# Kernel tuning notes

Hardware: AMD Instinct MI355X
Metric: run time of the kernel (lower is better)

The kernel has to match this reference:

```python
import jax, jax.numpy as jnp
import numpy as np

ALPHA = 0.2          # LeakyReLU slope
COUNTER_COEFF = 0.5  # config.counter_coeff
N = 50000
E = 500000
NFEATS = 256
NHIDS = 256
NHEADS = 8
DH = NHIDS // NHEADS


def _gat_multihead(x_src, x_dst, src, dst, W, b, a_s, a_d, a_b, n_dst):
    """Multi-head GAT: gather-linear-leakyrelu edge attention, segment softmax,
    softmax-weighted scatter sum.  W:[H,F,D] b:[H,D] a_s,a_d:[H,D] a_b:[H].
    Returns [n_dst, H*D] (heads concatenated, as torch.cat over heads)."""
    Wh_s = jnp.einsum('nf,hfd->nhd', x_src, W) + b  # [Ns,H,D]
    Wh_d = jnp.einsum('nf,hfd->nhd', x_dst, W) + b  # [Nd,H,D]
    # a([Wh_src;Wh_dst]) decomposes into src and dst halves of the weight
    es = jnp.einsum('nhd,hd->nh', Wh_s, a_s)
    ed = jnp.einsum('nhd,hd->nh', Wh_d, a_d)
    e = jax.nn.leaky_relu(es[src] + ed[dst] + a_b, ALPHA)  # [E,H]
    # per-destination (mailbox) softmax, numerically stable
    emax = jax.ops.segment_max(e, dst, num_segments=n_dst)
    emax = jnp.where(jnp.isfinite(emax), emax, 0.0)
    ex = jnp.exp(e - emax[dst])
    denom = jax.ops.segment_sum(ex, dst, num_segments=n_dst)
    att = ex / denom[dst]                          # every edge's dst has >=1 edge
    msg = att[:, :, None] * Wh_s[src]              # [E,H,D]
    out = jax.ops.segment_sum(msg, dst, num_segments=n_dst)  # [n_dst,H,D]
    return out.reshape(n_dst, -1)


def _gru_cell(x, h, W_ih, W_hh, b_ih, b_hh):
    gi = x @ W_ih.T + b_ih
    gh = h @ W_hh.T + b_hh
    i_r, i_z, i_n = jnp.split(gi, 3, axis=1)
    h_r, h_z, h_n = jnp.split(gh, 3, axis=1)
    r = jax.nn.sigmoid(i_r + h_r)
    z = jax.nn.sigmoid(i_z + h_z)
    n = jnp.tanh(i_n + r * h_n)
    return (1.0 - z) * n + z * h


def setup_inputs() -> dict:
    key = jax.random.key(0)
    ks = jax.random.split(key, 20)
    xavier = lambda k, shape, fin, fout: jax.random.uniform(
        k, shape, jnp.float32, -1.0, 1.0) * (1.414 * np.sqrt(6.0 / (fin + fout)))
    inp = {}
    inp['h'] = jax.random.normal(ks[0], (N, NFEATS), jnp.float32)
    inp['hp_counter'] = jax.random.normal(ks[1], (N, NHIDS), jnp.float32)
    inp['hp_support'] = jax.random.normal(ks[2], (N, NHIDS), jnp.float32)
    inp['hp_dst'] = jax.random.normal(ks[3], (N, NHIDS), jnp.float32)
    # intra-turn GAT weights (per head)
    inp['W_gat'] = xavier(ks[4], (NHEADS, NFEATS, DH), NFEATS, DH)
    inp['b_gat'] = jnp.zeros((NHEADS, DH), jnp.float32)
    inp['as_gat'] = xavier(ks[5], (NHEADS, DH), 2 * DH, 1)
    inp['ad_gat'] = xavier(ks[6], (NHEADS, DH), 2 * DH, 1)
    inp['ab_gat'] = jnp.zeros((NHEADS,), jnp.float32)
    # cross-turn GAT weights (shared for counter & support: same self.xgat)
    inp['W_x'] = xavier(ks[7], (NHEADS, NHIDS, DH), NHIDS, DH)
    inp['b_x'] = jnp.zeros((NHEADS, DH), jnp.float32)
    inp['as_x'] = xavier(ks[8], (NHEADS, DH), 2 * DH, 1)
    inp['ad_x'] = xavier(ks[9], (NHEADS, DH), 2 * DH, 1)
    inp['ab_x'] = jnp.zeros((NHEADS,), jnp.float32)
    # GRUCell(nhids, nhids)
    s = 1.0 / np.sqrt(NHIDS)
    inp['W_ih'] = jax.random.uniform(ks[10], (3 * NHIDS, NHIDS), jnp.float32, -s, s)
    inp['W_hh'] = jax.random.uniform(ks[11], (3 * NHIDS, NHIDS), jnp.float32, -s, s)
    inp['b_ih'] = jax.random.uniform(ks[12], (3 * NHIDS,), jnp.float32, -s, s)
    inp['b_hh'] = jax.random.uniform(ks[13], (3 * NHIDS,), jnp.float32, -s, s)
    # edge lists
    inp['edge_src'] = jax.random.randint(ks[14], (E,), 0, N, jnp.int32)
    inp['edge_dst'] = jax.random.randint(ks[15], (E,), 0, N, jnp.int32)
    inp['edge_c_src'] = jax.random.randint(ks[16], (E,), 0, N, jnp.int32)
    inp['edge_c_dst'] = jax.random.randint(ks[17], (E,), 0, N, jnp.int32)
    inp['edge_s_src'] = jax.random.randint(ks[18], (E,), 0, N, jnp.int32)
    inp['edge_s_dst'] = jax.random.randint(ks[19], (E,), 0, N, jnp.int32)
    return inp


def reference(h, hp_counter, hp_support, hp_dst,
              W_gat, b_gat, as_gat, ad_gat, ab_gat,
              W_x, b_x, as_x, ad_x, ab_x,
              W_ih, W_hh, b_ih, b_hh,
              edge_src, edge_dst, edge_c_src, edge_c_dst,
              edge_s_src, edge_s_dst):
    # x = self.gat(g, t): intra-turn multi-head GAT on raw features h
    x = _gat_multihead(h, h, edge_src, edge_dst,
                       W_gat, b_gat, as_gat, ad_gat, ab_gat, N)
    # h_c = self.xgat(g, t-1, 'counter'): directed GAT, prev-turn -> current
    h_c = _gat_multihead(hp_counter, hp_dst, edge_c_src, edge_c_dst,
                         W_x, b_x, as_x, ad_x, ab_x, N)
    # h_s = self.xgat(g, t-2, 'support') (same weights)
    h_s = _gat_multihead(hp_support, hp_dst, edge_s_src, edge_s_dst,
                         W_x, b_x, as_x, ad_x, ab_x, N)
    hmix = COUNTER_COEFF * h_c + (1.0 - COUNTER_COEFF) * h_s
    hprime = _gru_cell(x, hmix, W_ih, W_hh, b_ih, b_hh)
    return hprime
```

## Files before the change

kernel.cpp:

```cpp
#include <hip/hip_runtime.h>
#include <math.h>

#define ALPHA 0.2f
#define LOG2E 1.44269504088896f

constexpr int FEATS = 256;
constexpr int HEADS = 8;

typedef unsigned short u16;
typedef __attribute__((ext_vector_type(8))) short bf16x8;
typedef __attribute__((ext_vector_type(4))) float f32x4;

__device__ __forceinline__ u16 f2b(float f) {
    unsigned u = __float_as_uint(f);
    u += 0x7FFF + ((u >> 16) & 1);
    return (u16)(u >> 16);
}
__device__ __forceinline__ float b2f(u16 x) {
    return __uint_as_float(((unsigned)x) << 16);
}
__device__ __forceinline__ unsigned pk2(float lo, float hi) {
    return __builtin_amdgcn_perm(__float_as_uint(hi), __float_as_uint(lo), 0x07060302u);
}
__device__ __forceinline__ void gload16(const void* g, void* l) {
    __builtin_amdgcn_global_load_lds(
        (const __attribute__((address_space(1))) unsigned int*)g,
        (__attribute__((address_space(3))) unsigned int*)l, 16, 0, 0);
}
__device__ __forceinline__ float rsum16(float v) {
    v += __shfl_xor(v, 1); v += __shfl_xor(v, 2);
    v += __shfl_xor(v, 4); v += __shfl_xor(v, 8);
    return v;
}

__global__ void prep_count_kernel(
    const float* __restrict__ W_gat, const float* __restrict__ W_x,
    const float* __restrict__ W_ih, const float* __restrict__ W_hh,
    u16* __restrict__ Bgat, u16* __restrict__ Bx,
    u16* __restrict__ Bihr, u16* __restrict__ Bhhr,
    const int* __restrict__ d0, const int* __restrict__ d1,
    const int* __restrict__ d2, int* __restrict__ cnt, int E, int N) {
    int b = blockIdx.x;
    if (b < 2048) {
        int i = b * 256 + threadIdx.x;
        if (i < 131072) {
            int j = i & 65535;
            int n = j >> 8, f = j & 255;
            int h2 = n >> 5, d = n & 31;
            const float* W = (i < 65536) ? W_gat : W_x;
            u16* Bt = (i < 65536) ? Bgat : Bx;
            Bt[j] = f2b(W[(h2 * 256 + f) * 32 + d]);
        } else {
            int x = i - 131072;
            int lin = (x < 196608) ? x : x - 196608;
            int c = lin >> 8, k = lin & 255;
            int q = c / 48, rr = c - q * 48;
            int g = rr >> 4, jl = rr & 15;
            int orig = (g * 256 + q * 16 + jl) * 256 + k;
            if (x < 196608) Bihr[lin] = f2b(W_ih[orig]);
            else            Bhhr[lin] = f2b(W_hh[orig]);
        }
    } else {
        int i = (b - 2048) * 256 + threadIdx.x;
        if (i >= 3 * E) return;
        if (i < E) atomicAdd(&cnt[d0[i]], 1);
        else if (i < 2 * E) atomicAdd(&cnt[N + d1[i - E]], 1);
        else atomicAdd(&cnt[2 * N + d2[i - 2 * E]], 1);
    }
}

__global__ void scan1_kernel(const int* __restrict__ cnt, int* __restrict__ off,
                             int* __restrict__ blksum, int n) {
    __shared__ int tmp[256];
    int t = threadIdx.x;
    int base = blockIdx.x * 1024 + t * 4;
    int v[4];
#pragma unroll
    for (int k = 0; k < 4; ++k) v[k] = (base + k < n) ? cnt[base + k] : 0;
    int s = v[0] + v[1] + v[2] + v[3];
    tmp[t] = s;
    __syncthreads();
    for (int st = 1; st < 256; st <<= 1) {
        int add = (t >= st) ? tmp[t - st] : 0;
        __syncthreads();
        tmp[t] += add;
        __syncthreads();
    }
    int ex = tmp[t] - s;
#pragma unroll
    for (int k = 0; k < 4; ++k) {
        if (base + k < n) off[base + k] = ex;
        ex += v[k];
    }
    if (t == 255) blksum[blockIdx.x] = tmp[255];
}
__global__ void scan2_kernel(int* __restrict__ blksum, int nb) {
    __shared__ int tmp[256];
    int t = threadIdx.x;
    int v = (t < nb) ? blksum[t] : 0;
    tmp[t] = v;
    __syncthreads();
    for (int s = 1; s < 256; s <<= 1) {
        int add = (t >= s) ? tmp[t - s] : 0;
        __syncthreads();
        tmp[t] += add;
        __syncthreads();
    }
    if (t < nb) blksum[t] = tmp[t] - v;
}
__global__ void scan3_kernel(int* __restrict__ off, int* __restrict__ cur,
                             const int* __restrict__ blksum, int n) {
    int i = blockIdx.x * blockDim.x + threadIdx.x;
    if (i < n) {
        int v = off[i] + blksum[i >> 10];
        off[i] = v;
        cur[i] = v;
    }
}

__global__ void fill3_kernel(const int* __restrict__ s0, const int* __restrict__ d0,
                             const int* __restrict__ s1, const int* __restrict__ d1,
                             const int* __restrict__ s2, const int* __restrict__ d2,
                             int* __restrict__ cur, int* __restrict__ srcs, int E, int N) {
    int i = blockIdx.x * blockDim.x + threadIdx.x;
    if (i >= 3 * E) return;
    int s, slot;
    if (i < E) { s = s0[i]; slot = d0[i]; }
    else if (i < 2 * E) { s = s1[i - E]; slot = N + d1[i - E]; }
    else { s = s2[i - 2 * E]; slot = 2 * N + d2[i - 2 * E]; }
    int p = atomicAdd(&cur[slot], 1);
    srcs[p] = s;
}

__global__ __launch_bounds__(512, 4) void proj4_kernel(
    const float* __restrict__ A0, const float* __restrict__ A1,
    const float* __restrict__ A2, const float* __restrict__ A3,
    const u16* __restrict__ Bg, const u16* __restrict__ Bx,
    const float* __restrict__ bg, const float* __restrict__ bx,
    u16* __restrict__ C0, u16* __restrict__ C1,
    u16* __restrict__ C2, u16* __restrict__ C3,
    const float* __restrict__ as_g, const float* __restrict__ ad_g,
    const float* __restrict__ as_x, const float* __restrict__ ad_x,
    float* __restrict__ es1, float* __restrict__ ed1,
    float* __restrict__ esC, float* __restrict__ edD,
    float* __restrict__ esS,
    int M, int NB) {
    __shared__ char As_raw[32768];
    __shared__ char Bs_raw[32768];
    const int tid = threadIdx.x;
    const int lane = tid & 63;
    const int wid = tid >> 6;
    const int wr = wid >> 2, wc = wid & 3;
    const int seg = blockIdx.x / NB;
    const int bm = (blockIdx.x % NB) * 128;
    const int l15 = lane & 15;
    const float* A = (seg == 0) ? A0 : (seg == 1) ? A1 : (seg == 2) ? A2 : A3;
    const u16* B = (seg == 0) ? Bg : Bx;
    const float* bias = (seg == 0) ? bg : bx;
    u16* C = (seg == 0) ? C0 : (seg == 1) ? C1 : (seg == 2) ? C2 : C3;
    const float* asP = (seg == 0) ? as_g : (seg == 2) ? nullptr : as_x;
    const float* adP = (seg == 0) ? ad_g : (seg == 2) ? ad_x : nullptr;
    float* esP = (seg == 0) ? es1 : (seg == 1) ? esC : (seg == 3) ? esS : nullptr;
    float* edP = (seg == 0) ? ed1 : (seg == 2) ? edD : nullptr;

    f32x4 acc[4][4];
#pragma unroll
    for (int m = 0; m < 4; ++m)
#pragma unroll
        for (int n = 0; n < 4; ++n) acc[m][n] = (f32x4)0.f;

    for (int kb = 0; kb < 4; ++kb) {
        const int k0g = kb * 64;
#pragma unroll
        for (int i = 0; i < 4; ++i) {
            int s = i * 512 + tid;
            int row = s >> 4, c16 = s & 15;
            int gr = min(bm + row, M - 1);
            int gcol = k0g + ((c16 ^ (row & 7)) << 2);
            gload16(A + (size_t)gr * 256 + gcol, As_raw + s * 16);
        }
#pragma unroll
        for (int i = 0; i < 4; ++i) {
            int s = i * 512 + tid;
            int row = s >> 3, c16 = s & 7;
            int gcol = k0g + (c16 ^ (row & 7)) * 8;
            gload16(B + (size_t)row * 256 + gcol, Bs_raw + s * 16);
        }
        __syncthreads();
#pragma unroll
        for (int kk = 0; kk < 2; ++kk) {
            const int kc = (kk * 32 + (lane >> 4) * 8) >> 3;
            bf16x8 af[4], bfr[4];
#pragma unroll
            for (int m = 0; m < 4; ++m) {
                int row = wr * 64 + m * 16 + l15;
                int r7 = row & 7;
                int u0 = (2 * kc) ^ r7;
                f32x4 lo = *(const f32x4*)(As_raw + row * 256 + u0 * 16);
                f32x4 hi = *(const f32x4*)(As_raw + row * 256 + (u0 ^ 1) * 16);
                union { unsigned u[4]; bf16x8 v; } cv;
                cv.u[0] = pk2(lo.x, lo.y); cv.u[1] = pk2(lo.z, lo.w);
                cv.u[2] = pk2(hi.x, hi.y); cv.u[3] = pk2(hi.z, hi.w);
                af[m] = cv.v;
            }
#pragma unroll
            for (int n = 0; n < 4; ++n) {
                int row = wc * 64 + n * 16 + l15;
                bfr[n] = *(const bf16x8*)(Bs_raw + row * 128 + ((kc ^ (row & 7)) << 4));
            }
#pragma unroll
            for (int m = 0; m < 4; ++m)
#pragma unroll
                for (int n = 0; n < 4; ++n)
                    acc[m][n] = __builtin_amdgcn_mfma_f32_16x16x32_bf16(
                        af[m], bfr[n], acc[m][n], 0, 0, 0);
        }
        __syncthreads();
    }
    const int hb = wc * 2;
    float cS[4], cD[4];
#pragma unroll
    for (int n = 0; n < 4; ++n) {
        int hn = hb + (n >> 1);
        int ix = (n & 1) * 16 + l15;
        cS[n] = asP ? asP[hn * 32 + ix] : 0.f;
        cD[n] = adP ? adP[hn * 32 + ix] : 0.f;
    }
#pragma unroll
    for (int m = 0; m < 4; ++m) {
#pragma unroll
        for (int j = 0; j < 4; ++j) {
            int gr = bm + wr * 64 + m * 16 + (lane >> 4) * 4 + j;
            float tmp[4];
#pragma unroll
            for (int n = 0; n < 4; ++n)
                tmp[n] = acc[m][n][j] + bias[wc * 64 + n * 16 + l15];
            if (gr < M) {
#pragma unroll
                for (int n = 0; n < 4; ++n)
                    C[(size_t)gr * 256 + wc * 64 + n * 16 + l15] = f2b(tmp[n]);
            }
#pragma unroll
            for (int g = 0; g < 2; ++g) {
                if (esP) {
                    float ps = cS[2 * g] * tmp[2 * g] + cS[2 * g + 1] * tmp[2 * g + 1];
                    ps = rsum16(ps);
                    if (l15 == 0 && gr < M) esP[(size_t)gr * 8 + hb + g] = ps * LOG2E;
                }
                if (edP) {
                    float pd = cD[2 * g] * tmp[2 * g] + cD[2 * g + 1] * tmp[2 * g + 1];
                    pd = rsum16(pd);
                    if (l15 == 0 && gr < M) edP[(size_t)gr * 8 + hb + g] = pd * LOG2E;
                }
            }
        }
    }
}

__device__ __forceinline__ void run_seg(
    const int* __restrict__ srcs, int start, int deg,
    const float* __restrict__ es, const u16* __restrict__ Wh,
    float edv, int o, int hh,
    float& psum, float4& a) {
    psum = 0.f;
    a = make_float4(0.f, 0.f, 0.f, 0.f);
    if (deg <= 0) return;
    int sP = srcs[start];
    int sN = (deg > 1) ? srcs[start + 1] : sP;
    float rawP = es[sP * 8 + hh];
    ushort4 wP = *(const ushort4*)(Wh + (size_t)sP * FEATS + o);
    for (int j = 0; j < deg; ++j) {
        int sNN = (j + 2 < deg) ? srcs[start + j + 2] : sN;
        float rawN = es[sN * 8 + hh];
        ushort4 wN = *(const ushort4*)(Wh + (size_t)sN * FEATS + o);
        float e = rawP + edv;
        e = e > 0.f ? e : ALPHA * e;
        float pe = exp2f(e);
        psum += pe;
        a.x += pe * b2f(wP.x);
        a.y += pe * b2f(wP.y);
        a.z += pe * b2f(wP.z);
        a.w += pe * b2f(wP.w);
        rawP = rawN; wP = wN; sN = sNN;
    }
}

__global__ __launch_bounds__(256) void gather_all_kernel(
    const int* __restrict__ off, const int* __restrict__ cnt,
    const int* __restrict__ srcs,
    const float* __restrict__ es1, const float* __restrict__ ed1,
    const float* __restrict__ esC, const float* __restrict__ edD,
    const float* __restrict__ esS,
    const float* __restrict__ ab_g, const float* __restrict__ ab_x,
    const u16* __restrict__ Wh1, const u16* __restrict__ WhC,
    const u16* __restrict__ WhS3,
    u16* __restrict__ xb, u16* __restrict__ hmixb, int N) {
    int gwid = (blockIdx.x * blockDim.x + threadIdx.x) >> 6;
    if (gwid >= 2 * N) return;
    int lane = threadIdx.x & 63;
    int o = lane * 4, hh = lane >> 3;
    if (gwid < N) {
        int node = gwid;
        float edv = ed1[node * 8 + hh] + ab_g[hh] * LOG2E;
        float psum; float4 a;
        run_seg(srcs, off[node], cnt[node], es1, Wh1, edv, o, hh, psum, a);
        float sc = (cnt[node] > 0) ? (1.0f / psum) : 0.f;
        ushort4 r;
        r.x = f2b(a.x * sc); r.y = f2b(a.y * sc);
        r.z = f2b(a.z * sc); r.w = f2b(a.w * sc);
        *(ushort4*)(xb + (size_t)node * FEATS + o) = r;
    } else {
        int node = gwid - N;
        float edv = edD[node * 8 + hh] + ab_x[hh] * LOG2E;
        int st2 = off[N + node],     dg2 = cnt[N + node];
        int st3 = off[2 * N + node], dg3 = cnt[2 * N + node];
        float ps2, ps3;
        float4 a2, a3;
        if (dg2 > 0 && dg3 > 0) {
            ps2 = 0.f; ps3 = 0.f;
            a2 = make_float4(0.f, 0.f, 0.f, 0.f);
            a3 = make_float4(0.f, 0.f, 0.f, 0.f);
            int sP2 = srcs[st2];
            int sN2 = (dg2 > 1) ? srcs[st2 + 1] : sP2;
            float r2 = esC[sP2 * 8 + hh];
            ushort4 w2 = *(const ushort4*)(WhC + (size_t)sP2 * FEATS + o);
            int sP3 = srcs[st3];
            int sN3 = (dg3 > 1) ? srcs[st3 + 1] : sP3;
            float r3 = esS[sP3 * 8 + hh];
            ushort4 w3 = *(const ushort4*)(WhS3 + (size_t)sP3 * FEATS + o);
            int j2 = 0, j3 = 0;
            const int c = min(dg2, dg3);
            for (int t = 0; t < c; ++t) {
                int sNN2 = (j2 + 2 < dg2) ? srcs[st2 + j2 + 2] : sN2;
                float rn2 = esC[sN2 * 8 + hh];
                ushort4 wn2 = *(const ushort4*)(WhC + (size_t)sN2 * FEATS + o);
                int sNN3 = (j3 + 2 < dg3) ? srcs[st3 + j3 + 2] : sN3;
                float rn3 = esS[sN3 * 8 + hh];
                ushort4 wn3 = *(const ushort4*)(WhS3 + (size_t)sN3 * FEATS + o);
                float e2 = r2 + edv; e2 = e2 > 0.f ? e2 : ALPHA * e2;
                float p2 = exp2f(e2);
                ps2 += p2;
                a2.x += p2 * b2f(w2.x); a2.y += p2 * b2f(w2.y);
                a2.z += p2 * b2f(w2.z); a2.w += p2 * b2f(w2.w);
                float e3 = r3 + edv; e3 = e3 > 0.f ? e3 : ALPHA * e3;
                float p3 = exp2f(e3);
                ps3 += p3;
                a3.x += p3 * b2f(w3.x); a3.y += p3 * b2f(w3.y);
                a3.z += p3 * b2f(w3.z); a3.w += p3 * b2f(w3.w);
                r2 = rn2; w2 = wn2; sN2 = sNN2; ++j2;
                r3 = rn3; w3 = wn3; sN3 = sNN3; ++j3;
            }
            for (; j2 < dg2; ++j2) {
                int sNN2 = (j2 + 2 < dg2) ? srcs[st2 + j2 + 2] : sN2;
                float rn2 = esC[sN2 * 8 + hh];
                ushort4 wn2 = *(const ushort4*)(WhC + (size_t)sN2 * FEATS + o);
                float e2 = r2 + edv; e2 = e2 > 0.f ? e2 : ALPHA * e2;
                float p2 = exp2f(e2);
                ps2 += p2;
                a2.x += p2 * b2f(w2.x); a2.y += p2 * b2f(w2.y);
                a2.z += p2 * b2f(w2.z); a2.w += p2 * b2f(w2.w);
                r2 = rn2; w2 = wn2; sN2 = sNN2;
            }
            for (; j3 < dg3; ++j3) {
                int sNN3 = (j3 + 2 < dg3) ? srcs[st3 + j3 + 2] : sN3;
                float rn3 = esS[sN3 * 8 + hh];
                ushort4 wn3 = *(const ushort4*)(WhS3 + (size_t)sN3 * FEATS + o);
                float e3 = r3 + edv; e3 = e3 > 0.f ? e3 : ALPHA * e3;
                float p3 = exp2f(e3);
                ps3 += p3;
                a3.x += p3 * b2f(w3.x); a3.y += p3 * b2f(w3.y);
                a3.z += p3 * b2f(w3.z); a3.w += p3 * b2f(w3.w);
                r3 = rn3; w3 = wn3; sN3 = sNN3;
            }
        } else {
            run_seg(srcs, st2, dg2, esC, WhC, edv, o, hh, ps2, a2);
            run_seg(srcs, st3, dg3, esS, WhS3, edv, o, hh, ps3, a3);
        }
        float sc2 = (dg2 > 0) ? (0.5f / ps2) : 0.f;
        float sc3 = (dg3 > 0) ? (0.5f / ps3) : 0.f;
        ushort4 r;
        r.x = f2b(a2.x * sc2 + a3.x * sc3);
        r.y = f2b(a2.y * sc2 + a3.y * sc3);
        r.z = f2b(a2.z * sc2 + a3.z * sc3);
        r.w = f2b(a2.w * sc2 + a3.w * sc3);
        *(ushort4*)(hmixb + (size_t)node * FEATS + o) = r;
    }
}

__global__ __launch_bounds__(512, 4) void gru_fused_kernel(
    const u16* __restrict__ xb, const u16* __restrict__ hmixb,
    const u16* __restrict__ Bihr, const u16* __restrict__ Bhhr,
    const float* __restrict__ b_ih, const float* __restrict__ b_hh,
    float* __restrict__ out, int M) {
    __shared__ char As[16384];
    __shared__ char Bs[24576];
    const int tid = threadIdx.x;
    const int lane = tid & 63;
    const int wid = tid >> 6;
    const int wr = wid >> 2, wq = wid & 3;
    const int bt = blockIdx.x;
    const int bm = blockIdx.y * 128;
    const int l15 = lane & 15;

    f32x4 acc[4][3], acc2[4];
#pragma unroll
    for (int m = 0; m < 4; ++m) {
#pragma unroll
        for (int g = 0; g < 3; ++g) acc[m][g] = (f32x4)0.f;
        acc2[m] = (f32x4)0.f;
    }

#pragma unroll
    for (int pass = 0; pass < 2; ++pass) {
        const u16* A = pass ? hmixb : xb;
        const u16* B = pass ? Bhhr : Bihr;
        for (int kb = 0; kb < 4; ++kb) {
            const int k0g = kb * 64;
#pragma unroll
            for (int i = 0; i < 2; ++i) {
                int s = i * 512 + tid;
                int row = s >> 3, c16 = s & 7;
                int gr = min(bm + row, M - 1);
                int gcol = k0g + (c16 ^ (row & 7)) * 8;
                gload16(A + (size_t)gr * 256 + gcol, As + s * 16);
            }
#pragma unroll
            for (int i = 0; i < 3; ++i) {
                int s = i * 512 + tid;
                int row = s >> 3, c16 = s & 7;
                int gcol = k0g + (c16 ^ (row & 7)) * 8;
                gload16(B + (size_t)(bt * 192 + row) * 256 + gcol, Bs + s * 16);
            }
            __syncthreads();
#pragma unroll
            for (int kk = 0; kk < 2; ++kk) {
                const int kc = (kk * 32 + (lane >> 4) * 8) >> 3;
                bf16x8 af[4], bfr[3];
#pragma unroll
                for (int m = 0; m < 4; ++m) {
                    int row = wr * 64 + m * 16 + l15;
                    af[m] = *(const bf16x8*)(As + row * 128 + ((kc ^ (row & 7)) << 4));
                }
#pragma unroll
                for (int g = 0; g < 3; ++g) {
                    int row = wq * 48 + g * 16 + l15;
                    bfr[g] = *(const bf16x8*)(Bs + row * 128 + ((kc ^ (row & 7)) << 4));
                }
#pragma unroll
                for (int m = 0; m < 4; ++m) {
#pragma unroll
                    for (int g = 0; g < 3; ++g) {
                        if (pass == 1 && g == 2)
                            acc2[m] = __builtin_amdgcn_mfma_f32_16x16x32_bf16(
                                af[m], bfr[g], acc2[m], 0, 0, 0);
                        else
                            acc[m][g] = __builtin_amdgcn_mfma_f32_16x16x32_bf16(
                                af[m], bfr[g], acc[m][g], 0, 0, 0);
                    }
                }
            }
            __syncthreads();
        }
    }
    const int j = (bt * 4 + wq) * 16 + l15;
    const float bir = b_ih[j], biz = b_ih[256 + j], bin = b_ih[512 + j];
    const float bhr = b_hh[j], bhz = b_hh[256 + j], bhn = b_hh[512 + j];
#pragma unroll
    for (int m = 0; m < 4; ++m) {
#pragma unroll
        for (int jj = 0; jj < 4; ++jj) {
            int row = bm + wr * 64 + m * 16 + (lane >> 4) * 4 + jj;
            if (row < M) {
                float gr_ = acc[m][0][jj] + bir + bhr;
                float gz_ = acc[m][1][jj] + biz + bhz;
                float rr = 1.f / (1.f + exp2f(-gr_ * LOG2E));
                float zz = 1.f / (1.f + exp2f(-gz_ * LOG2E));
                float nn = tanhf(acc[m][2][jj] + bin + rr * (acc2[m][jj] + bhn));
                float hm = b2f(hmixb[(size_t)row * 256 + j]);
                out[(size_t)row * 256 + j] = (1.f - zz) * nn + zz * hm;
            }
        }
    }
}

extern "C" void kernel_launch(void* const* d_in, const int* in_sizes, int n_in,
                              void* d_out, int out_size, void* d_ws, size_t ws_size,
                              hipStream_t stream) {
    const float* h        = (const float*)d_in[0];
    const float* hp_cnt   = (const float*)d_in[1];
    const float* hp_sup   = (const float*)d_in[2];
    const float* hp_dst   = (const float*)d_in[3];
    const float* W_gat    = (const float*)d_in[4];
    const float* b_gat    = (const float*)d_in[5];
    const float* as_gat   = (const float*)d_in[6];
    const float* ad_gat   = (const float*)d_in[7];
    const float* ab_gat   = (const float*)d_in[8];
    const float* W_x      = (const float*)d_in[9];
    const float* b_x      = (const float*)d_in[10];
    const float* as_x     = (const float*)d_in[11];
    const float* ad_x     = (const float*)d_in[12];
    const float* ab_x     = (const float*)d_in[13];
    const float* W_ih     = (const float*)d_in[14];
    const float* W_hh     = (const float*)d_in[15];
    const float* b_ih     = (const float*)d_in[16];
    const float* b_hh     = (const float*)d_in[17];
    const int* e_src      = (const int*)d_in[18];
    const int* e_dst      = (const int*)d_in[19];
    const int* ec_src     = (const int*)d_in[20];
    const int* ec_dst     = (const int*)d_in[21];
    const int* es_src     = (const int*)d_in[22];
    const int* es_dst     = (const int*)d_in[23];

    const int N = in_sizes[0] / FEATS;
    const int E = in_sizes[18];
    const int N8 = N * HEADS;
    const int N3 = 3 * N;
    const int NBLK3 = (N3 + 1023) / 1024;
    const int NB128 = (N + 127) / 128;

    char* ws = (char*)d_ws;
    size_t p = 0;
    u16* Wh1   = (u16*)(ws + p); p += (size_t)N * FEATS * 2;
    u16* WhC   = (u16*)(ws + p); p += (size_t)N * FEATS * 2;
    u16* WhD   = (u16*)(ws + p); p += (size_t)N * FEATS * 2;
    u16* WhS3  = (u16*)(ws + p); p += (size_t)N * FEATS * 2;
    u16* xb    = (u16*)(ws + p); p += (size_t)N * FEATS * 2;
    u16* hmixb = (u16*)(ws + p); p += (size_t)N * FEATS * 2;
    float* es1 = (float*)(ws + p); p += (size_t)N8 * 4;
    float* ed1 = (float*)(ws + p); p += (size_t)N8 * 4;
    float* esC = (float*)(ws + p); p += (size_t)N8 * 4;
    float* edD = (float*)(ws + p); p += (size_t)N8 * 4;
    float* esS = (float*)(ws + p); p += (size_t)N8 * 4;
    int* cnt3  = (int*)(ws + p); p += (size_t)N3 * 4;
    int* off3  = (int*)(ws + p); p += (size_t)N3 * 4;
    int* cur3  = (int*)(ws + p); p += (size_t)N3 * 4;
    int* blks  = (int*)(ws + p); p += 1024;
    int* srcs3 = (int*)(ws + p); p += (size_t)3 * E * 4;
    u16* Bgat  = (u16*)(ws + p); p += 65536 * 2;
    u16* Bx    = (u16*)(ws + p); p += 65536 * 2;
    u16* Bihr  = (u16*)(ws + p); p += 196608 * 2;
    u16* Bhhr  = (u16*)(ws + p); p += 196608 * 2;

    const dim3 blk(256);
    const dim3 blk512(512);
    const int g3E256 = (3 * E + 255) / 256;

    hipMemsetAsync(cnt3, 0, (size_t)N3 * 4, stream);
    prep_count_kernel<<<2048 + g3E256, blk, 0, stream>>>(
        W_gat, W_x, W_ih, W_hh, Bgat, Bx, Bihr, Bhhr,
        e_dst, ec_dst, es_dst, cnt3, E, N);

    scan1_kernel<<<NBLK3, blk, 0, stream>>>(cnt3, off3, blks, N3);
    scan2_kernel<<<1, blk, 0, stream>>>(blks, NBLK3);
    scan3_kernel<<<(N3 + 255) / 256, blk, 0, stream>>>(off3, cur3, blks, N3);

    fill3_kernel<<<g3E256, blk, 0, stream>>>(e_src, e_dst, ec_src, ec_dst,
                                             es_src, es_dst, cur3, srcs3, E, N);

    proj4_kernel<<<4 * NB128, blk512, 0, stream>>>(
        h, hp_cnt, hp_dst, hp_sup, Bgat, Bx, b_gat, b_x,
        Wh1, WhC, WhD, WhS3,
        as_gat, ad_gat, as_x, ad_x,
        es1, ed1, esC, edD, esS, N, NB128);

    gather_all_kernel<<<(2 * N * 64 + 255) / 256, blk, 0, stream>>>(
        off3, cnt3, srcs3, es1, ed1, esC, edD, esS, ab_gat, ab_x,
        Wh1, WhC, WhS3, xb, hmixb, N);

    gru_fused_kernel<<<dim3(4, NB128), blk512, 0, stream>>>(
        xb, hmixb, Bihr, Bhhr, b_ih, b_hh, (float*)d_out, N);
}
```

Baseline: 484.6 us.

## Double-buffer LDS tiles in projection and GRU GEMMs with K=32 stages

Both GEMM kernels (proj4 and gru_fused) now use two LDS buffers and smaller K-steps of 32. The next tile's global-to-LDS load is issued before computing on the current one, so load latency overlaps with MFMA work and each step needs one barrier instead of two. The swizzle patterns are reworked for the narrower 64/128-byte rows. The trade-off is more loop iterations and barriers with less work per step, plus a changed bank-conflict pattern.

```diff
diff --git a/kernel.cpp b/kernel.cpp
--- a/kernel.cpp
+++ b/kernel.cpp
@@ -145,8 +145,8 @@
     float* __restrict__ esC, float* __restrict__ edD,
     float* __restrict__ esS,
     int M, int NB) {
-    __shared__ char As_raw[32768];
-    __shared__ char Bs_raw[32768];
+    __shared__ char As_raw[2][16384];
+    __shared__ char Bs_raw[2][16384];
     const int tid = threadIdx.x;
     const int lane = tid & 63;
     const int wid = tid >> 6;
@@ -169,52 +169,55 @@
 #pragma unroll
         for (int n = 0; n < 4; ++n) acc[m][n] = (f32x4)0.f;
 
-    for (int kb = 0; kb < 4; ++kb) {
-        const int k0g = kb * 64;
-#pragma unroll
-        for (int i = 0; i < 4; ++i) {
+    auto STAGE = [&](int buf, int kb) {
+        const int k0g = kb * 32;
+#pragma unroll
+        for (int i = 0; i < 2; ++i) {
             int s = i * 512 + tid;
-            int row = s >> 4, c16 = s & 15;
+            int row = s >> 3, c8 = s & 7;
             int gr = min(bm + row, M - 1);
-            int gcol = k0g + ((c16 ^ (row & 7)) << 2);
-            gload16(A + (size_t)gr * 256 + gcol, As_raw + s * 16);
-        }
-#pragma unroll
-        for (int i = 0; i < 4; ++i) {
+            int gcol = k0g + ((c8 ^ (row & 7)) << 2);
+            gload16(A + (size_t)gr * 256 + gcol, As_raw[buf] + s * 16);
+        }
+#pragma unroll
+        for (int i = 0; i < 2; ++i) {
             int s = i * 512 + tid;
-            int row = s >> 3, c16 = s & 7;
-            int gcol = k0g + (c16 ^ (row & 7)) * 8;
-            gload16(B + (size_t)row * 256 + gcol, Bs_raw + s * 16);
-        }
-        __syncthreads();
-#pragma unroll
-        for (int kk = 0; kk < 2; ++kk) {
-            const int kc = (kk * 32 + (lane >> 4) * 8) >> 3;
-            bf16x8 af[4], bfr[4];
-#pragma unroll
-            for (int m = 0; m < 4; ++m) {
-                int row = wr * 64 + m * 16 + l15;
-                int r7 = row & 7;
-                int u0 = (2 * kc) ^ r7;
-                f32x4 lo = *(const f32x4*)(As_raw + row * 256 + u0 * 16);
-                f32x4 hi = *(const f32x4*)(As_raw + row * 256 + (u0 ^ 1) * 16);
-                union { unsigned u[4]; bf16x8 v; } cv;
-                cv.u[0] = pk2(lo.x, lo.y); cv.u[1] = pk2(lo.z, lo.w);
-                cv.u[2] = pk2(hi.x, hi.y); cv.u[3] = pk2(hi.z, hi.w);
-                af[m] = cv.v;
-            }
-#pragma unroll
-            for (int n = 0; n < 4; ++n) {
-                int row = wc * 64 + n * 16 + l15;
-                bfr[n] = *(const bf16x8*)(Bs_raw + row * 128 + ((kc ^ (row & 7)) << 4));
-            }
-#pragma unroll
-            for (int m = 0; m < 4; ++m)
-#pragma unroll
-                for (int n = 0; n < 4; ++n)
-                    acc[m][n] = __builtin_amdgcn_mfma_f32_16x16x32_bf16(
-                        af[m], bfr[n], acc[m][n], 0, 0, 0);
-        }
+            int row = s >> 2, c4 = s & 3;
+            int gcol = k0g + (c4 ^ ((row >> 1) & 3)) * 8;
+            gload16(B + (size_t)row * 256 + gcol, Bs_raw[buf] + s * 16);
+        }
+    };
+
+    STAGE(0, 0);
+    __syncthreads();
+    for (int kb = 0; kb < 8; ++kb) {
+        const int cur = kb & 1;
+        if (kb < 7) STAGE(cur ^ 1, kb + 1);
+        const int kc = lane >> 4;
+        bf16x8 af[4], bfr[4];
+#pragma unroll
+        for (int m = 0; m < 4; ++m) {
+            int row = wr * 64 + m * 16 + l15;
+            int u0 = (2 * kc) ^ (row & 7);
+            f32x4 lo = *(const f32x4*)(As_raw[cur] + row * 128 + u0 * 16);
+            f32x4 hi = *(const f32x4*)(As_raw[cur] + row * 128 + (u0 ^ 1) * 16);
+            union { unsigned u[4]; bf16x8 v; } cv;
+            cv.u[0] = pk2(lo.x, lo.y); cv.u[1] = pk2(lo.z, lo.w);
+            cv.u[2] = pk2(hi.x, hi.y); cv.u[3] = pk2(hi.z, hi.w);
+            af[m] = cv.v;
+        }
+#pragma unroll
+        for (int n = 0; n < 4; ++n) {
+            int row = wc * 64 + n * 16 + l15;
+            bfr[n] = *(const bf16x8*)(Bs_raw[cur] + row * 64 +
+                                      ((kc ^ ((row >> 1) & 3)) << 4));
+        }
+#pragma unroll
+        for (int m = 0; m < 4; ++m)
+#pragma unroll
+            for (int n = 0; n < 4; ++n)
+                acc[m][n] = __builtin_amdgcn_mfma_f32_16x16x32_bf16(
+                    af[m], bfr[n], acc[m][n], 0, 0, 0);
         __syncthreads();
     }
     const int hb = wc * 2;
@@ -392,8 +395,8 @@
     const u16* __restrict__ Bihr, const u16* __restrict__ Bhhr,
     const float* __restrict__ b_ih, const float* __restrict__ b_hh,
     float* __restrict__ out, int M) {
-    __shared__ char As[16384];
-    __shared__ char Bs[24576];
+    __shared__ char As[2][8192];
+    __shared__ char Bs[2][12288];
     const int tid = threadIdx.x;
     const int lane = tid & 63;
     const int wid = tid >> 6;
@@ -410,57 +413,62 @@
         acc2[m] = (f32x4)0.f;
     }
 
-#pragma unroll
-    for (int pass = 0; pass < 2; ++pass) {
+    auto STAGE = [&](int buf, int t) {
+        const int pass = t >> 3, kb = t & 7;
         const u16* A = pass ? hmixb : xb;
         const u16* B = pass ? Bhhr : Bihr;
-        for (int kb = 0; kb < 4; ++kb) {
-            const int k0g = kb * 64;
-#pragma unroll
-            for (int i = 0; i < 2; ++i) {
-                int s = i * 512 + tid;
-                int row = s >> 3, c16 = s & 7;
-                int gr = min(bm + row, M - 1);
-                int gcol = k0g + (c16 ^ (row & 7)) * 8;
-                gload16(A + (size_t)gr * 256 + gcol, As + s * 16);
-            }
-#pragma unroll
-            for (int i = 0; i < 3; ++i) {
-                int s = i * 512 + tid;
-                int row = s >> 3, c16 = s & 7;
-                int gcol = k0g + (c16 ^ (row & 7)) * 8;
-                gload16(B + (size_t)(bt * 192 + row) * 256 + gcol, Bs + s * 16);
-            }
-            __syncthreads();
-#pragma unroll
-            for (int kk = 0; kk < 2; ++kk) {
-                const int kc = (kk * 32 + (lane >> 4) * 8) >> 3;
-                bf16x8 af[4], bfr[3];
-#pragma unroll
-                for (int m = 0; m < 4; ++m) {
-                    int row = wr * 64 + m * 16 + l15;
-                    af[m] = *(const bf16x8*)(As + row * 128 + ((kc ^ (row & 7)) << 4));
-                }
-#pragma unroll
-                for (int g = 0; g < 3; ++g) {
-                    int row = wq * 48 + g * 16 + l15;
-                    bfr[g] = *(const bf16x8*)(Bs + row * 128 + ((kc ^ (row & 7)) << 4));
-                }
-#pragma unroll
-                for (int m = 0; m < 4; ++m) {
-#pragma unroll
-                    for (int g = 0; g < 3; ++g) {
-                        if (pass == 1 && g == 2)
-                            acc2[m] = __builtin_amdgcn_mfma_f32_16x16x32_bf16(
-                                af[m], bfr[g], acc2[m], 0, 0, 0);
-                        else
-                            acc[m][g] = __builtin_amdgcn_mfma_f32_16x16x32_bf16(
-                                af[m], bfr[g], acc[m][g], 0, 0, 0);
-                    }
-                }
-            }
-            __syncthreads();
-        }
+        const int k0g = kb * 32;
+        {
+            int s = tid;
+            int row = s >> 2, c4 = s & 3;
+            int gr = min(bm + row, M - 1);
+            int gcol = k0g + (c4 ^ ((row >> 1) & 3)) * 8;
+            gload16(A + (size_t)gr * 256 + gcol, As[buf] + s * 16);
+        }
+#pragma unroll
+        for (int i = 0; i < 2; ++i) {
+            int s = i * 512 + tid;
+            if (s < 768) {
+                int row = s >> 2, c4 = s & 3;
+                int gcol = k0g + (c4 ^ ((row >> 1) & 3)) * 8;
+                gload16(B + (size_t)(bt * 192 + row) * 256 + gcol, Bs[buf] + s * 16);
+            }
+        }
+    };
+
+    STAGE(0, 0);
+    __syncthreads();
+    for (int t = 0; t < 16; ++t) {
+        const int cur = t & 1;
+        if (t < 15) STAGE(cur ^ 1, t + 1);
+        const int pass = t >> 3;
+        const int kc = lane >> 4;
+        bf16x8 af[4], bfr[3];
+#pragma unroll
+        for (int m = 0; m < 4; ++m) {
+            int row = wr * 64 + m * 16 + l15;
+            af[m] = *(const bf16x8*)(As[cur] + row * 64 +
+                                     ((kc ^ ((row >> 1) & 3)) << 4));
+        }
+#pragma unroll
+        for (int g = 0; g < 3; ++g) {
+            int row = wq * 48 + g * 16 + l15;
+            bfr[g] = *(const bf16x8*)(Bs[cur] + row * 64 +
+                                      ((kc ^ ((row >> 1) & 3)) << 4));
+        }
+#pragma unroll
+        for (int m = 0; m < 4; ++m) {
+#pragma unroll
+            for (int g = 0; g < 3; ++g) {
+                if (pass == 1 && g == 2)
+                    acc2[m] = __builtin_amdgcn_mfma_f32_16x16x32_bf16(
+                        af[m], bfr[g], acc2[m], 0, 0, 0);
+                else
+                    acc[m][g] = __builtin_amdgcn_mfma_f32_16x16x32_bf16(
+                        af[m], bfr[g], acc[m][g], 0, 0, 0);
+            }
+        }
+        __syncthreads();
     }
     const int j = (bt * 4 + wq) * 16 + l15;
     const float bir = b_ih[j], biz = b_ih[256 + j], bin = b_ih[512 + j];
```

Measured after the change: 486.7 us. No clear change (+0.4%).
